# Kernel optimization log

Hardware: AMD Instinct MI355X
Metric: run time of the kernel (lower is better)

## Reference

```python
import jax, jax.numpy as jnp
import numpy as np

B, N_IN, D_IN = 2048, 49, 320
D = 768            # inner_dim
H = 8              # n_heads
DH = D // H        # head dim = 96
NQ = 8             # n_queries
D_OUT = 3072       # llama_hidden
EPS = 1e-5


def _ln(x, g, b):
    mu = jnp.mean(x, axis=-1, keepdims=True)
    var = jnp.mean(jnp.square(x - mu), axis=-1, keepdims=True)
    return (x - mu) * jax.lax.rsqrt(var + EPS) * g + b


def setup_inputs() -> dict:
    key = jax.random.key(0)
    ks = jax.random.split(key, 16)
    s = lambda k, shape, fan: jax.random.normal(k, shape, jnp.float32) * (1.0 / np.sqrt(fan))
    return {
        "features": jax.random.normal(ks[0], (B, N_IN, D_IN), jnp.float32),
        "input_proj_w": s(ks[1], (D, D_IN), D_IN),
        "input_proj_b": jnp.zeros((D,), jnp.float32),
        "queries": jax.random.normal(ks[2], (NQ, D), jnp.float32) * 0.02,
        "ln_q_g": jnp.ones((D,), jnp.float32), "ln_q_b": jnp.zeros((D,), jnp.float32),
        "ln_kv_g": jnp.ones((D,), jnp.float32), "ln_kv_b": jnp.zeros((D,), jnp.float32),
        "in_proj_w": s(ks[3], (3 * D, D), D),
        "in_proj_b": jnp.zeros((3 * D,), jnp.float32),
        "out_proj_w": s(ks[4], (D, D), D),
        "out_proj_b": jnp.zeros((D,), jnp.float32),
        "ln_ff_g": jnp.ones((D,), jnp.float32), "ln_ff_b": jnp.zeros((D,), jnp.float32),
        "ffn_w1": s(ks[5], (D, D), D), "ffn_b1": jnp.zeros((D,), jnp.float32),
        "ffn_w2": s(ks[6], (D, D), D), "ffn_b2": jnp.zeros((D,), jnp.float32),
        "output_proj_w": s(ks[7], (D_OUT, D), D),
        "output_proj_b": jnp.zeros((D_OUT,), jnp.float32),
        "final_g": jnp.ones((D_OUT,), jnp.float32), "final_b": jnp.zeros((D_OUT,), jnp.float32),
    }


def reference(features, input_proj_w, input_proj_b, queries,
              ln_q_g, ln_q_b, ln_kv_g, ln_kv_b,
              in_proj_w, in_proj_b, out_proj_w, out_proj_b,
              ln_ff_g, ln_ff_b, ffn_w1, ffn_b1, ffn_w2, ffn_b2,
              output_proj_w, output_proj_b, final_g, final_b):
    b = features.shape[0]
    # kv projection: (B, N_in, D)
    kv = jnp.einsum('bnd,ed->bne', features, input_proj_w) + input_proj_b
    q = jnp.broadcast_to(queries[None], (b, NQ, D))

    # --- single layer (n_layers=1) ---
    q_norm = _ln(q, ln_q_g, ln_q_b)
    kv_norm = _ln(kv, ln_kv_g, ln_kv_b)

    wq, wk, wv = in_proj_w[:D], in_proj_w[D:2 * D], in_proj_w[2 * D:]
    bq, bk, bv = in_proj_b[:D], in_proj_b[D:2 * D], in_proj_b[2 * D:]
    qp = (jnp.einsum('bqd,ed->bqe', q_norm, wq) + bq).reshape(b, NQ, H, DH)
    kp = (jnp.einsum('bnd,ed->bne', kv_norm, wk) + bk).reshape(b, N_IN, H, DH)
    vp = (jnp.einsum('bnd,ed->bne', kv_norm, wv) + bv).reshape(b, N_IN, H, DH)

    scores = jnp.einsum('bqhd,bnhd->bhqn', qp, kp) / np.sqrt(DH).astype(np.float32)
    attn = jax.nn.softmax(scores, axis=-1)
    ctx = jnp.einsum('bhqn,bnhd->bqhd', attn, vp).reshape(b, NQ, D)
    attn_out = jnp.einsum('bqd,ed->bqe', ctx, out_proj_w) + out_proj_b

    q = q + attn_out
    h = _ln(q, ln_ff_g, ln_ff_b)
    h = jnp.einsum('bqd,ed->bqe', h, ffn_w1) + ffn_b1
    h = jax.nn.gelu(h, approximate=False)
    h = jnp.einsum('bqd,ed->bqe', h, ffn_w2) + ffn_b2
    q = q + h

    out = jnp.einsum('bqd,ed->bqe', q, output_proj_w) + output_proj_b
    return _ln(out, final_g, final_b)
```

## Files before the change

kernel.cpp:

```cpp
#include <hip/hip_runtime.h>
#include <math.h>

typedef __attribute__((ext_vector_type(8))) short short8;
typedef __attribute__((ext_vector_type(8))) unsigned short ushort8;
typedef __attribute__((ext_vector_type(4))) float f32x4;

__device__ __forceinline__ float b2f(unsigned short h) {
    union { unsigned int u; float f; } c; c.u = ((unsigned int)h) << 16; return c.f;
}
__device__ __forceinline__ unsigned short f2b(float x) {
    union { float f; unsigned int u; } c; c.f = x;
    unsigned int r = c.u + 0x7fffu + ((c.u >> 16) & 1u);
    return (unsigned short)(r >> 16);
}

__global__ __launch_bounds__(256) void cast_all(
    const float* __restrict__ f,    unsigned short* __restrict__ fb,
    const float* __restrict__ winw, unsigned short* __restrict__ winb,
    const float* __restrict__ wv,   unsigned short* __restrict__ wvb,
    const float* __restrict__ wo,   unsigned short* __restrict__ wob,
    const float* __restrict__ w1,   unsigned short* __restrict__ w1b,
    const float* __restrict__ w2,   unsigned short* __restrict__ w2b,
    const float* __restrict__ wop,  unsigned short* __restrict__ wopb) {
    int blk = blockIdx.x;
    const float* src; unsigned short* dst; int i;
    if (blk < 31360)      { src = f;    dst = fb;   i = blk * 256 + threadIdx.x; }
    else if (blk < 31600) { src = winw; dst = winb; i = (blk - 31360) * 256 + threadIdx.x; }
    else if (blk < 32176) { src = wv;   dst = wvb;  i = (blk - 31600) * 256 + threadIdx.x; }
    else if (blk < 32752) { src = wo;   dst = wob;  i = (blk - 32176) * 256 + threadIdx.x; }
    else if (blk < 33328) { src = w1;   dst = w1b;  i = (blk - 32752) * 256 + threadIdx.x; }
    else if (blk < 33904) { src = w2;   dst = w2b;  i = (blk - 33328) * 256 + threadIdx.x; }
    else                  { src = wop;  dst = wopb; i = (blk - 33904) * 256 + threadIdx.x; }
    float4 fv = ((const float4*)src)[i];
    ushort4 o; o.x = f2b(fv.x); o.y = f2b(fv.y); o.z = f2b(fv.z); o.w = f2b(fv.w);
    ((ushort4*)dst)[i] = o;
}

template <int DD, bool INB, bool OUTB>
__global__ __launch_bounds__(256) void ln_rows(const void* __restrict__ in_, void* __restrict__ out_,
                                               const float* __restrict__ g, const float* __restrict__ bb,
                                               int nrows) {
    const int wv = threadIdx.x >> 6, l = threadIdx.x & 63;
    const int row = blockIdx.x * 4 + wv;
    if (row >= nrows) return;
    constexpr int NC = DD / 256;
    float v[DD / 64];
    if constexpr (INB) {
        const ushort4* in = (const ushort4*)((const unsigned short*)in_ + (size_t)row * DD);
#pragma unroll
        for (int c = 0; c < NC; ++c) {
            ushort4 u = in[l + 64 * c];
            v[4*c] = b2f(u.x); v[4*c+1] = b2f(u.y); v[4*c+2] = b2f(u.z); v[4*c+3] = b2f(u.w);
        }
    } else {
        const float4* in = (const float4*)((const float*)in_ + (size_t)row * DD);
#pragma unroll
        for (int c = 0; c < NC; ++c) {
            float4 u = in[l + 64 * c];
            v[4*c] = u.x; v[4*c+1] = u.y; v[4*c+2] = u.z; v[4*c+3] = u.w;
        }
    }
    float s = 0.f, s2 = 0.f;
#pragma unroll
    for (int i = 0; i < DD / 64; ++i) { s += v[i]; s2 += v[i] * v[i]; }
#pragma unroll
    for (int o = 32; o > 0; o >>= 1) { s += __shfl_xor(s, o, 64); s2 += __shfl_xor(s2, o, 64); }
    const float mu = s * (1.0f / DD);
    const float var = s2 * (1.0f / DD) - mu * mu;
    const float rs = rsqrtf(var + 1e-5f);
    if constexpr (OUTB) {
        ushort4* out = (ushort4*)((unsigned short*)out_ + (size_t)row * DD);
#pragma unroll
        for (int c = 0; c < NC; ++c) {
            int e = (l + 64 * c) * 4;
            ushort4 o4;
            o4.x = f2b((v[4*c]   - mu) * rs * g[e]   + bb[e]);
            o4.y = f2b((v[4*c+1] - mu) * rs * g[e+1] + bb[e+1]);
            o4.z = f2b((v[4*c+2] - mu) * rs * g[e+2] + bb[e+2]);
            o4.w = f2b((v[4*c+3] - mu) * rs * g[e+3] + bb[e+3]);
            out[l + 64 * c] = o4;
        }
    } else {
        float4* out = (float4*)((float*)out_ + (size_t)row * DD);
#pragma unroll
        for (int c = 0; c < NC; ++c) {
            int e = (l + 64 * c) * 4;
            float4 o4;
            o4.x = (v[4*c]   - mu) * rs * g[e]   + bb[e];
            o4.y = (v[4*c+1] - mu) * rs * g[e+1] + bb[e+1];
            o4.z = (v[4*c+2] - mu) * rs * g[e+2] + bb[e+2];
            o4.w = (v[4*c+3] - mu) * rs * g[e+3] + bb[e+3];
            out[l + 64 * c] = o4;
        }
    }
}

__global__ __launch_bounds__(256) void ln_stats(const unsigned short* __restrict__ kv,
                                                float2* __restrict__ stats, int nrows) {
    const int wv = threadIdx.x >> 6, l = threadIdx.x & 63;
    const int row = blockIdx.x * 4 + wv;
    if (row >= nrows) return;
    const ushort4* in = (const ushort4*)(kv + (size_t)row * 768);
    float s = 0.f, s2 = 0.f;
#pragma unroll
    for (int c = 0; c < 3; ++c) {
        ushort4 u = in[l + 64 * c];
        float a = b2f(u.x), b = b2f(u.y), cc = b2f(u.z), d = b2f(u.w);
        s += a + b + cc + d;
        s2 += a * a + b * b + cc * cc + d * d;
    }
#pragma unroll
    for (int o = 32; o > 0; o >>= 1) { s += __shfl_xor(s, o, 64); s2 += __shfl_xor(s2, o, 64); }
    const float mu = s * (1.0f / 768.0f);
    const float var = s2 * (1.0f / 768.0f) - mu * mu;
    const float rs = rsqrtf(var + 1e-5f);
    if (l == 0) stats[row] = make_float2(rs, rs * mu);
}

__global__ __launch_bounds__(256) void qp_kernel(const float* __restrict__ qn, const float* __restrict__ wq,
                                                 const float* __restrict__ bq, float* __restrict__ qp) {
    int q = blockIdx.x / 3;
    int col = (blockIdx.x % 3) * 256 + threadIdx.x;
    const float4* a = (const float4*)(qn + q * 768);
    const float4* wr = (const float4*)(wq + (size_t)col * 768);
    float s = 0.f;
#pragma unroll 8
    for (int k = 0; k < 192; ++k) {
        float4 xx = a[k], yy = wr[k];
        s += xx.x * yy.x + xx.y * yy.y + xx.z * yy.z + xx.w * yy.w;
    }
    qp[q * 768 + col] = s + bq[col];
}

__global__ __launch_bounds__(256) void qk_build(const float* __restrict__ qp, const float* __restrict__ wk,
                                                const float* __restrict__ g,
                                                unsigned short* __restrict__ qkg, float* __restrict__ tout) {
    __shared__ float red[4];
    const int hq = blockIdx.x, h = hq >> 3, q = hq & 7;
    const int tid = threadIdx.x;
    const float* qv = qp + q * 768 + h * 96;
    float tsum = 0.f;
#pragma unroll
    for (int c = 0; c < 3; ++c) {
        int e = tid + 256 * c;
        float s = 0.f;
        for (int d = 0; d < 96; ++d) s += qv[d] * wk[(size_t)(h * 96 + d) * 768 + e];
        unsigned short bv = f2b(s * 0.10206207262f * g[e]);
        qkg[hq * 768 + e] = bv;
        tsum += b2f(bv);
    }
#pragma unroll
    for (int o = 32; o > 0; o >>= 1) tsum += __shfl_xor(tsum, o, 64);
    if ((tid & 63) == 0) red[tid >> 6] = tsum;
    __syncthreads();
    if (tid == 0) tout[hq] = red[0] + red[1] + red[2] + red[3];
}

__device__ __forceinline__ void gll16(const void* g, void* l) {
    __builtin_amdgcn_global_load_lds((const __attribute__((address_space(1))) unsigned int*)g,
                                     (__attribute__((address_space(3))) unsigned int*)l, 16, 0, 0);
}

template <int ROWS>
__device__ __forceinline__ void stage_rows(const unsigned short* gbase, int ldg,
                                           unsigned short* lds, int tid) {
    int wuni = tid & ~63;
#pragma unroll
    for (int it = 0; it < ROWS / 32; ++it) {
        int s = it * 256 + tid;
        int r = s >> 3, c = s & 7;
        int cc = c ^ (r & 7);
        gll16(gbase + (size_t)r * ldg + cc * 8, lds + (size_t)(it * 256 + wuni) * 8);
    }
}

template <int EPI>
__global__ __launch_bounds__(256) void gemm_bf16(
    const unsigned short* __restrict__ A, const unsigned short* __restrict__ W,
    const float* __restrict__ bias, void* __restrict__ out,
    const float* __restrict__ aux, int K, int N) {
    __shared__ __align__(16) unsigned short lA[128 * 64];
    __shared__ __align__(16) unsigned short lB[128 * 64];
    const int tid = threadIdx.x;
    const int l = tid & 63, w = tid >> 6;
    int gx = gridDim.x;
    int lid = blockIdx.y * gx + blockIdx.x;
    int nwg = gx * gridDim.y;
    int idx = (nwg & 7) ? lid : ((lid & 7) * (nwg >> 3) + (lid >> 3));
    const int bm0 = (idx / gx) * 128, bn0 = (idx % gx) * 128;
    const int wm = (w >> 1) * 64, wn = (w & 1) * 64;
    const int l15 = l & 15, lk = l >> 4;
    f32x4 acc[4][4] = {};
    const int nk = K >> 6;
    const unsigned short* Abase = A + (size_t)bm0 * K;
    const unsigned short* Wbase = W + (size_t)bn0 * K;
    for (int kt = 0; kt < nk; ++kt) {
        stage_rows<128>(Abase + kt * 64, K, lA, tid);
        stage_rows<128>(Wbase + kt * 64, K, lB, tid);
        __syncthreads();
        short8 af[4], bf[4];
#pragma unroll
        for (int kk = 0; kk < 2; ++kk) {
#pragma unroll
            for (int mf = 0; mf < 4; ++mf) {
                int r = wm + mf * 16 + l15;
                int c = (kk * 4 + lk) ^ (r & 7);
                af[mf] = *(const short8*)(lA + r * 64 + c * 8);
            }
#pragma unroll
            for (int nf = 0; nf < 4; ++nf) {
                int r = wn + nf * 16 + l15;
                int c = (kk * 4 + lk) ^ (r & 7);
                bf[nf] = *(const short8*)(lB + r * 64 + c * 8);
            }
#pragma unroll
            for (int mf = 0; mf < 4; ++mf)
#pragma unroll
                for (int nf = 0; nf < 4; ++nf)
                    acc[mf][nf] = __builtin_amdgcn_mfma_f32_16x16x32_bf16(af[mf], bf[nf], acc[mf][nf], 0, 0, 0);
        }
        __syncthreads();
    }
    const int row0 = bm0 + wm + (lk << 2);
    const int col0 = bn0 + wn + l15;
#pragma unroll
    for (int nf = 0; nf < 4; ++nf) {
        int col = col0 + nf * 16;
        float bv = bias[col];
#pragma unroll
        for (int mf = 0; mf < 4; ++mf) {
#pragma unroll
            for (int r = 0; r < 4; ++r) {
                int row = row0 + mf * 16 + r;
                float v = acc[mf][nf][r] + bv;
                size_t idx2 = (size_t)row * N + col;
                if constexpr (EPI == 0) {
                    ((unsigned short*)out)[idx2] = f2b(v);
                } else if constexpr (EPI == 1) {
                    v += aux[(row & 7) * N + col];
                    ((float*)out)[idx2] = v;
                } else if constexpr (EPI == 2) {
                    v = 0.5f * v * (1.0f + erff(v * 0.70710678118f));
                    ((unsigned short*)out)[idx2] = f2b(v);
                } else if constexpr (EPI == 3) {
                    v += aux[idx2];
                    ((unsigned short*)out)[idx2] = f2b(v);
                } else {
                    ((float*)out)[idx2] = v;
                }
            }
        }
    }
}

__global__ __launch_bounds__(256) void gemm_scores(const unsigned short* __restrict__ A,
                                                   const unsigned short* __restrict__ Qk,
                                                   const float2* __restrict__ stats,
                                                   const float* __restrict__ tcol,
                                                   float* __restrict__ S) {
    __shared__ __align__(16) unsigned short lA[128 * 64];
    __shared__ __align__(16) unsigned short lB[64 * 64];
    const int tid = threadIdx.x;
    const int l = tid & 63, w = tid >> 6;
    int lid = blockIdx.x;
    int idx = (lid & 7) * (gridDim.x >> 3) + (lid >> 3);
    const int bm0 = idx * 128;
    const int wm = (w >> 1) * 64, wn = (w & 1) * 32;
    const int l15 = l & 15, lk = l >> 4;
    f32x4 acc[4][2] = {};
    const unsigned short* Abase = A + (size_t)bm0 * 768;
    for (int kt = 0; kt < 12; ++kt) {
        stage_rows<128>(Abase + kt * 64, 768, lA, tid);
        stage_rows<64>(Qk + kt * 64, 768, lB, tid);
        __syncthreads();
        short8 af[4], bf[2];
#pragma unroll
        for (int kk = 0; kk < 2; ++kk) {
#pragma unroll
            for (int mf = 0; mf < 4; ++mf) {
                int r = wm + mf * 16 + l15;
                int c = (kk * 4 + lk) ^ (r & 7);
                af[mf] = *(const short8*)(lA + r * 64 + c * 8);
            }
#pragma unroll
            for (int nf = 0; nf < 2; ++nf) {
                int r = wn + nf * 16 + l15;
                int c = (kk * 4 + lk) ^ (r & 7);
                bf[nf] = *(const short8*)(lB + r * 64 + c * 8);
            }
#pragma unroll
            for (int mf = 0; mf < 4; ++mf)
#pragma unroll
                for (int nf = 0; nf < 2; ++nf)
                    acc[mf][nf] = __builtin_amdgcn_mfma_f32_16x16x32_bf16(af[mf], bf[nf], acc[mf][nf], 0, 0, 0);
        }
        __syncthreads();
    }
    const int row0 = bm0 + wm + (lk << 2);
    const int col0 = wn + l15;
    const float tv0 = tcol[col0], tv1 = tcol[col0 + 16];
#pragma unroll
    for (int mf = 0; mf < 4; ++mf)
#pragma unroll
        for (int r = 0; r < 4; ++r) {
            int row = row0 + mf * 16 + r;
            float2 st = stats[row];
            S[(size_t)row * 64 + col0]      = st.x * acc[mf][0][r] - st.y * tv0;
            S[(size_t)row * 64 + col0 + 16] = st.x * acc[mf][1][r] - st.y * tv1;
        }
}

__global__ __launch_bounds__(256) void attn_mix(const unsigned short* __restrict__ kvr,
                                                const float* __restrict__ S,
                                                const float2* __restrict__ stats,
                                                const float* __restrict__ lg,
                                                const float* __restrict__ lb,
                                                unsigned short* __restrict__ cmix) {
    __shared__ __align__(16) unsigned short at[64 * 64];
    __shared__ __align__(16) unsigned short kvT[128 * 64];
    __shared__ float dl[64];
    float* Sl = (float*)kvT;
    const int b = blockIdx.x;
    const int t = threadIdx.x, l = t & 63, w = t >> 6;
    const int l15 = l & 15, lk = l >> 4;

    for (int i = t; i < 3136; i += 256) Sl[i] = S[(size_t)b * 3136 + i];

    const unsigned short* src = kvr + ((size_t)b * 49 + (l < 49 ? l : 0)) * 768;
    ushort8 z8 = {0, 0, 0, 0, 0, 0, 0, 0};
    ushort8 va0 = z8, va1 = z8, va2 = z8, va3 = z8;
    if (l < 49) {
        va0 = *(const ushort8*)(src + w * 8);
        va1 = *(const ushort8*)(src + w * 8 + 32);
        va2 = *(const ushort8*)(src + w * 8 + 64);
        va3 = *(const ushort8*)(src + w * 8 + 96);
    }
    __syncthreads();

    float mx = -1e30f;
    for (int n = 0; n < 49; ++n) mx = fmaxf(mx, Sl[n * 64 + l]);
    float sum = 0.f, dun = 0.f;
    for (int n = 0; n < 49; ++n) {
        float e = __expf(Sl[n * 64 + l] - mx);
        sum += e;
        dun += e * stats[(size_t)b * 49 + n].y;
    }
    float inv = 1.0f / sum;
#pragma unroll
    for (int cd = 0; cd < 2; ++cd) {
        int c = w * 2 + cd;
        int cc = c ^ (l & 7);
#pragma unroll
        for (int j = 0; j < 8; ++j) {
            int n = c * 8 + j;
            float av = 0.f;
            if (n < 49) av = __expf(Sl[n * 64 + l] - mx) * inv * stats[(size_t)b * 49 + n].x;
            at[l * 64 + cc * 8 + j] = f2b(av);
        }
    }
    if (w == 0) dl[l] = dun * inv;
    __syncthreads();

    float dls[4];
#pragma unroll
    for (int nf = 0; nf < 4; ++nf) dls[nf] = dl[nf * 16 + l15];

#pragma unroll 1
    for (int ph = 0; ph < 6; ++ph) {
#pragma unroll
        for (int i = 0; i < 4; ++i) {
            ushort8 v = (i == 0) ? va0 : (i == 1) ? va1 : (i == 2) ? va2 : va3;
            int e0 = w * 8 + i * 32;
#pragma unroll
            for (int j = 0; j < 8; ++j) {
                int e = e0 + j;
                kvT[e * 64 + (((l >> 3) ^ (e & 7)) << 3) + (l & 7)] = v[j];
            }
        }
        ushort8 nb0 = z8, nb1 = z8, nb2 = z8, nb3 = z8;
        if (ph < 5 && l < 49) {
            const unsigned short* s2 = src + (ph + 1) * 128 + w * 8;
            nb0 = *(const ushort8*)(s2);
            nb1 = *(const ushort8*)(s2 + 32);
            nb2 = *(const ushort8*)(s2 + 64);
            nb3 = *(const ushort8*)(s2 + 96);
        }
        __syncthreads();
        f32x4 acc[2][4] = {};
#pragma unroll
        for (int ks = 0; ks < 2; ++ks) {
            short8 af[2], bf[4];
#pragma unroll
            for (int mf = 0; mf < 2; ++mf) {
                int r = w * 32 + mf * 16 + l15;
                af[mf] = *(const short8*)(kvT + r * 64 + (((ks * 4 + lk) ^ (r & 7)) << 3));
            }
#pragma unroll
            for (int nf = 0; nf < 4; ++nf) {
                int r = nf * 16 + l15;
                bf[nf] = *(const short8*)(at + r * 64 + (((ks * 4 + lk) ^ (r & 7)) << 3));
            }
#pragma unroll
            for (int mf = 0; mf < 2; ++mf)
#pragma unroll
                for (int nf = 0; nf < 4; ++nf)
                    acc[mf][nf] = __builtin_amdgcn_mfma_f32_16x16x32_bf16(af[mf], bf[nf], acc[mf][nf], 0, 0, 0);
        }
#pragma unroll
        for (int mf = 0; mf < 2; ++mf) {
            int e0 = ph * 128 + w * 32 + mf * 16 + lk * 4;
            float4 g4 = *(const float4*)(lg + e0);
            float4 b4 = *(const float4*)(lb + e0);
#pragma unroll
            for (int nf = 0; nf < 4; ++nf) {
                int hq = nf * 16 + l15;
                float dv = dls[nf];
                ushort4 o;
                o.x = f2b(g4.x * (acc[mf][nf][0] - dv) + b4.x);
                o.y = f2b(g4.y * (acc[mf][nf][1] - dv) + b4.y);
                o.z = f2b(g4.z * (acc[mf][nf][2] - dv) + b4.z);
                o.w = f2b(g4.w * (acc[mf][nf][3] - dv) + b4.w);
                *(ushort4*)(cmix + ((size_t)(hq >> 3) * 16384 + b * 8 + (hq & 7)) * 768 + e0) = o;
            }
        }
        va0 = nb0; va1 = nb1; va2 = nb2; va3 = nb3;
        __syncthreads();
    }
}

__global__ __launch_bounds__(256) void gemm_ctx(const unsigned short* __restrict__ cmix,
                                                const unsigned short* __restrict__ wvb,
                                                const float* __restrict__ bv,
                                                unsigned short* __restrict__ ctx) {
    __shared__ __align__(16) unsigned short lA[128 * 64];
    __shared__ __align__(16) unsigned short lB[128 * 64];
    const int tid = threadIdx.x;
    const int l = tid & 63, w = tid >> 6;
    const int h = blockIdx.z;
    int yy = blockIdx.y;
    int idx = (yy & 7) * 16 + (yy >> 3);
    const int bm0 = idx * 128;
    const int wm = (w >> 1) * 64, wn = (w & 1) * 64;
    const int l15 = l & 15, lk = l >> 4;
    f32x4 acc[4][4] = {};
    const unsigned short* Abase = cmix + (size_t)h * 16384 * 768 + (size_t)bm0 * 768;
    const unsigned short* Wbase = wvb + (size_t)h * 96 * 768;
    for (int kt = 0; kt < 12; ++kt) {
        stage_rows<128>(Abase + kt * 64, 768, lA, tid);
        stage_rows<128>(Wbase + kt * 64, 768, lB, tid);
        __syncthreads();
        short8 af[4], bf[4];
#pragma unroll
        for (int kk = 0; kk < 2; ++kk) {
#pragma unroll
            for (int mf = 0; mf < 4; ++mf) {
                int r = wm + mf * 16 + l15;
                int c = (kk * 4 + lk) ^ (r & 7);
                af[mf] = *(const short8*)(lA + r * 64 + c * 8);
            }
#pragma unroll
            for (int nf = 0; nf < 4; ++nf) {
                int r = wn + nf * 16 + l15;
                int c = (kk * 4 + lk) ^ (r & 7);
                bf[nf] = *(const short8*)(lB + r * 64 + c * 8);
            }
#pragma unroll
            for (int mf = 0; mf < 4; ++mf)
#pragma unroll
                for (int nf = 0; nf < 4; ++nf)
                    acc[mf][nf] = __builtin_amdgcn_mfma_f32_16x16x32_bf16(af[mf], bf[nf], acc[mf][nf], 0, 0, 0);
        }
        __syncthreads();
    }
    const int row0 = bm0 + wm + (lk << 2);
    const int col0 = wn + l15;
#pragma unroll
    for (int nf = 0; nf < 4; ++nf) {
        int col = col0 + nf * 16;
        if (col >= 96) continue;
        float bvv = bv[h * 96 + col];
#pragma unroll
        for (int mf = 0; mf < 4; ++mf)
#pragma unroll
            for (int r = 0; r < 4; ++r) {
                int row = row0 + mf * 16 + r;
                ctx[(size_t)row * 768 + h * 96 + col] = f2b(acc[mf][nf][r] + bvv);
            }
    }
}

extern "C" void kernel_launch(void* const* d_in, const int* in_sizes, int n_in,
                              void* d_out, int out_size, void* d_ws, size_t ws_size,
                              hipStream_t stream) {
    (void)in_sizes; (void)n_in; (void)out_size;
    const float* features      = (const float*)d_in[0];
    const float* input_proj_w  = (const float*)d_in[1];
    const float* input_proj_b  = (const float*)d_in[2];
    const float* queries       = (const float*)d_in[3];
    const float* ln_q_g        = (const float*)d_in[4];
    const float* ln_q_b        = (const float*)d_in[5];
    const float* ln_kv_g       = (const float*)d_in[6];
    const float* ln_kv_b       = (const float*)d_in[7];
    const float* in_proj_w     = (const float*)d_in[8];
    const float* in_proj_b     = (const float*)d_in[9];
    const float* out_proj_w    = (const float*)d_in[10];
    const float* out_proj_b    = (const float*)d_in[11];
    const float* ln_ff_g       = (const float*)d_in[12];
    const float* ln_ff_b       = (const float*)d_in[13];
    const float* ffn_w1        = (const float*)d_in[14];
    const float* ffn_b1        = (const float*)d_in[15];
    const float* ffn_w2        = (const float*)d_in[16];
    const float* ffn_b2        = (const float*)d_in[17];
    const float* output_proj_w = (const float*)d_in[18];
    const float* output_proj_b = (const float*)d_in[19];
    const float* final_g       = (const float*)d_in[20];
    const float* final_b       = (const float*)d_in[21];

    char* ws = (char*)d_ws;
    size_t off = 0;
    auto alloc = [&](size_t bytes) -> char* {
        char* r = ws + off; off += (bytes + 255) & ~(size_t)255; return r;
    };
    unsigned short* featb = (unsigned short*)alloc(100352ull * 320 * 2);
    unsigned short* kvbuf = (unsigned short*)alloc(100352ull * 768 * 2);
    unsigned short* cmix  = (unsigned short*)alloc(8ull * 16384 * 768 * 2);
    float*          S     = (float*)alloc(100352ull * 64 * 4);
    float2*         stats = (float2*)alloc(100352ull * 8);
    unsigned short* winb  = (unsigned short*)alloc(768ull * 320 * 2);
    unsigned short* wvb   = (unsigned short*)alloc(768ull * 768 * 2);
    unsigned short* woutb = (unsigned short*)alloc(768ull * 768 * 2);
    unsigned short* w1b   = (unsigned short*)alloc(768ull * 768 * 2);
    unsigned short* w2b   = (unsigned short*)alloc(768ull * 768 * 2);
    unsigned short* wopb  = (unsigned short*)alloc(3072ull * 768 * 2);
    float* qnorm          = (float*)alloc(8 * 768 * 4);
    float* qpb            = (float*)alloc(8 * 768 * 4);
    unsigned short* qkb   = (unsigned short*)alloc(64ull * 768 * 2);
    float* tbuf           = (float*)alloc(64 * 4);
    if (off > ws_size) return;

    unsigned short* ctx  = featb;
    unsigned short* outb = kvbuf;
    float* x             = (float*)cmix;
    unsigned short* hn   = (unsigned short*)((char*)cmix + 50331648);
    unsigned short* f1   = (unsigned short*)((char*)cmix + 75497472);
    unsigned short* x2   = (unsigned short*)((char*)cmix + 100663296);

    cast_all<<<36208, 256, 0, stream>>>(features, featb, input_proj_w, winb,
                                        in_proj_w + 2 * 768 * 768, wvb, out_proj_w, woutb,
                                        ffn_w1, w1b, ffn_w2, w2b, output_proj_w, wopb);

    ln_rows<768, false, false><<<2, 256, 0, stream>>>(queries, qnorm, ln_q_g, ln_q_b, 8);
    qp_kernel<<<24, 256, 0, stream>>>(qnorm, in_proj_w, in_proj_b, qpb);
    qk_build<<<64, 256, 0, stream>>>(qpb, in_proj_w + 768 * 768, ln_kv_g, qkb, tbuf);

    gemm_bf16<0><<<dim3(6, 784), 256, 0, stream>>>(featb, winb, input_proj_b, kvbuf, nullptr, 320, 768);
    ln_stats<<<25088, 256, 0, stream>>>(kvbuf, stats, 100352);
    gemm_scores<<<784, 256, 0, stream>>>(kvbuf, qkb, stats, tbuf, S);
    attn_mix<<<2048, 256, 0, stream>>>(kvbuf, S, stats, ln_kv_g, ln_kv_b, cmix);
    gemm_ctx<<<dim3(1, 128, 8), 256, 0, stream>>>(cmix, wvb, in_proj_b + 1536, ctx);
    gemm_bf16<1><<<dim3(6, 128), 256, 0, stream>>>(ctx, woutb, out_proj_b, x, queries, 768, 768);
    ln_rows<768, false, true><<<4096, 256, 0, stream>>>(x, hn, ln_ff_g, ln_ff_b, 16384);
    gemm_bf16<2><<<dim3(6, 128), 256, 0, stream>>>(hn, w1b, ffn_b1, f1, nullptr, 768, 768);
    gemm_bf16<3><<<dim3(6, 128), 256, 0, stream>>>(f1, w2b, ffn_b2, x2, x, 768, 768);
    gemm_bf16<0><<<dim3(24, 128), 256, 0, stream>>>(x2, wopb, output_proj_b, outb, nullptr, 768, 3072);
    ln_rows<3072, true, false><<<4096, 256, 0, stream>>>(outb, (float*)d_out, final_g, final_b, 16384);
}
```

Baseline: 734.9 us.

## Fuse LayerNorm statistics into GEMM epilogues and fold FFN LN into W1

```diff
diff --git a/kernel.cpp b/kernel.cpp
--- a/kernel.cpp
+++ b/kernel.cpp
@@ -21,7 +21,8 @@
     const float* __restrict__ wo,   unsigned short* __restrict__ wob,
     const float* __restrict__ w1,   unsigned short* __restrict__ w1b,
     const float* __restrict__ w2,   unsigned short* __restrict__ w2b,
-    const float* __restrict__ wop,  unsigned short* __restrict__ wopb) {
+    const float* __restrict__ wop,  unsigned short* __restrict__ wopb,
+    const float* __restrict__ gff) {
     int blk = blockIdx.x;
     const float* src; unsigned short* dst; int i;
     if (blk < 31360)      { src = f;    dst = fb;   i = blk * 256 + threadIdx.x; }
@@ -32,6 +33,10 @@
     else if (blk < 33904) { src = w2;   dst = w2b;  i = (blk - 33328) * 256 + threadIdx.x; }
     else                  { src = wop;  dst = wopb; i = (blk - 33904) * 256 + threadIdx.x; }
     float4 fv = ((const float4*)src)[i];
+    if (blk >= 32752 && blk < 33328) {
+        float4 g4 = ((const float4*)gff)[i % 192];
+        fv.x *= g4.x; fv.y *= g4.y; fv.z *= g4.z; fv.w *= g4.w;
+    }
     ushort4 o; o.x = f2b(fv.x); o.y = f2b(fv.y); o.z = f2b(fv.z); o.w = f2b(fv.w);
     ((ushort4*)dst)[i] = o;
 }
@@ -95,28 +100,6 @@
     }
 }
 
-__global__ __launch_bounds__(256) void ln_stats(const unsigned short* __restrict__ kv,
-                                                float2* __restrict__ stats, int nrows) {
-    const int wv = threadIdx.x >> 6, l = threadIdx.x & 63;
-    const int row = blockIdx.x * 4 + wv;
-    if (row >= nrows) return;
-    const ushort4* in = (const ushort4*)(kv + (size_t)row * 768);
-    float s = 0.f, s2 = 0.f;
-#pragma unroll
-    for (int c = 0; c < 3; ++c) {
-        ushort4 u = in[l + 64 * c];
-        float a = b2f(u.x), b = b2f(u.y), cc = b2f(u.z), d = b2f(u.w);
-        s += a + b + cc + d;
-        s2 += a * a + b * b + cc * cc + d * d;
-    }
-#pragma unroll
-    for (int o = 32; o > 0; o >>= 1) { s += __shfl_xor(s, o, 64); s2 += __shfl_xor(s2, o, 64); }
-    const float mu = s * (1.0f / 768.0f);
-    const float var = s2 * (1.0f / 768.0f) - mu * mu;
-    const float rs = rsqrtf(var + 1e-5f);
-    if (l == 0) stats[row] = make_float2(rs, rs * mu);
-}
-
 __global__ __launch_bounds__(256) void qp_kernel(const float* __restrict__ qn, const float* __restrict__ wq,
                                                  const float* __restrict__ bq, float* __restrict__ qp) {
     int q = blockIdx.x / 3;
@@ -156,6 +139,24 @@
     if (tid == 0) tout[hq] = red[0] + red[1] + red[2] + red[3];
 }
 
+__global__ __launch_bounds__(256) void t1c1_build(const float* __restrict__ w1, const float* __restrict__ g,
+                                                  const float* __restrict__ beta, const float* __restrict__ b1,
+                                                  float* __restrict__ tvec, float* __restrict__ fb1) {
+    int col = blockIdx.x * 256 + threadIdx.x;
+    const float4* wr = (const float4*)(w1 + (size_t)col * 768);
+    const float4* g4 = (const float4*)g;
+    const float4* be = (const float4*)beta;
+    float st = 0.f, sc = 0.f;
+#pragma unroll 8
+    for (int k = 0; k < 192; ++k) {
+        float4 w = wr[k], gg = g4[k], bb = be[k];
+        st += w.x * gg.x + w.y * gg.y + w.z * gg.z + w.w * gg.w;
+        sc += w.x * bb.x + w.y * bb.y + w.z * bb.z + w.w * bb.w;
+    }
+    tvec[col] = st;
+    fb1[col] = sc + b1[col];
+}
+
 __device__ __forceinline__ void gll16(const void* g, void* l) {
     __builtin_amdgcn_global_load_lds((const __attribute__((address_space(1))) unsigned int*)g,
                                      (__attribute__((address_space(3))) unsigned int*)l, 16, 0, 0);
@@ -174,20 +175,31 @@
     }
 }
 
-template <int EPI>
+template <int EPI, bool STATS>
 __global__ __launch_bounds__(256) void gemm_bf16(
     const unsigned short* __restrict__ A, const unsigned short* __restrict__ W,
     const float* __restrict__ bias, void* __restrict__ out,
-    const float* __restrict__ aux, int K, int N) {
+    const void* __restrict__ aux, const float2* __restrict__ rstats,
+    float2* __restrict__ statsout, const float* __restrict__ tvec,
+    int K, int N, int CG) {
     __shared__ __align__(16) unsigned short lA[128 * 64];
     __shared__ __align__(16) unsigned short lB[128 * 64];
     const int tid = threadIdx.x;
     const int l = tid & 63, w = tid >> 6;
-    int gx = gridDim.x;
+    int gx = gridDim.x, gy = gridDim.y;
     int lid = blockIdx.y * gx + blockIdx.x;
-    int nwg = gx * gridDim.y;
-    int idx = (nwg & 7) ? lid : ((lid & 7) * (nwg >> 3) + (lid >> 3));
-    const int bm0 = (idx / gx) * 128, bn0 = (idx % gx) * 128;
+    int nwg = gx * gy;
+    int bm0, bn0;
+    if ((nwg & 7) || (gy & 7)) {
+        bm0 = (lid / gx) * 128; bn0 = (lid % gx) * 128;
+    } else {
+        int xcd = lid & 7, loc = lid >> 3;
+        int rpx = gy >> 3;
+        int perg = rpx * CG;
+        int cg = loc / perg, rem = loc % perg;
+        bm0 = (xcd * rpx + rem / CG) * 128;
+        bn0 = (cg * CG + rem % CG) * 128;
+    }
     const int wm = (w >> 1) * 64, wn = (w & 1) * 64;
     const int l15 = l & 15, lk = l >> 4;
     f32x4 acc[4][4] = {};
@@ -223,30 +235,53 @@
     }
     const int row0 = bm0 + wm + (lk << 2);
     const int col0 = bn0 + wn + l15;
+    float bv[4], tv[4];
 #pragma unroll
     for (int nf = 0; nf < 4; ++nf) {
-        int col = col0 + nf * 16;
-        float bv = bias[col];
-#pragma unroll
-        for (int mf = 0; mf < 4; ++mf) {
-#pragma unroll
-            for (int r = 0; r < 4; ++r) {
-                int row = row0 + mf * 16 + r;
-                float v = acc[mf][nf][r] + bv;
+        bv[nf] = bias[col0 + nf * 16];
+        if constexpr (EPI == 2) tv[nf] = tvec[col0 + nf * 16];
+    }
+#pragma unroll
+    for (int mf = 0; mf < 4; ++mf) {
+#pragma unroll
+        for (int r = 0; r < 4; ++r) {
+            int row = row0 + mf * 16 + r;
+            float rs = 0.f, u = 0.f;
+            if constexpr (EPI == 2) {
+                float2 sm = rstats[row];
+                float mu = sm.x * (1.0f / 768.0f);
+                float var = sm.y * (1.0f / 768.0f) - mu * mu;
+                rs = rsqrtf(var + 1e-5f);
+                u = rs * mu;
+            }
+            float smv = 0.f, smv2 = 0.f;
+#pragma unroll
+            for (int nf = 0; nf < 4; ++nf) {
+                int col = col0 + nf * 16;
                 size_t idx2 = (size_t)row * N + col;
+                float v = acc[mf][nf][r];
                 if constexpr (EPI == 0) {
-                    ((unsigned short*)out)[idx2] = f2b(v);
+                    v += bv[nf];
                 } else if constexpr (EPI == 1) {
-                    v += aux[(row & 7) * N + col];
-                    ((float*)out)[idx2] = v;
+                    v += bv[nf] + ((const float*)aux)[(row & 7) * N + col];
                 } else if constexpr (EPI == 2) {
+                    v = rs * v - u * tv[nf] + bv[nf];
                     v = 0.5f * v * (1.0f + erff(v * 0.70710678118f));
-                    ((unsigned short*)out)[idx2] = f2b(v);
-                } else if constexpr (EPI == 3) {
-                    v += aux[idx2];
-                    ((unsigned short*)out)[idx2] = f2b(v);
                 } else {
-                    ((float*)out)[idx2] = v;
+                    v += bv[nf] + b2f(((const unsigned short*)aux)[idx2]);
+                }
+                if constexpr (STATS) { smv += v; smv2 += v * v; }
+                ((unsigned short*)out)[idx2] = f2b(v);
+            }
+            if constexpr (STATS) {
+#pragma unroll
+                for (int o = 8; o > 0; o >>= 1) {
+                    smv += __shfl_xor(smv, o, 64);
+                    smv2 += __shfl_xor(smv2, o, 64);
+                }
+                if (l15 == 0) {
+                    atomicAdd(&((float*)statsout)[row * 2], smv);
+                    atomicAdd(&((float*)statsout)[row * 2 + 1], smv2);
                 }
             }
         }
@@ -304,9 +339,13 @@
 #pragma unroll
         for (int r = 0; r < 4; ++r) {
             int row = row0 + mf * 16 + r;
-            float2 st = stats[row];
-            S[(size_t)row * 64 + col0]      = st.x * acc[mf][0][r] - st.y * tv0;
-            S[(size_t)row * 64 + col0 + 16] = st.x * acc[mf][1][r] - st.y * tv1;
+            float2 sm = stats[row];
+            float mu = sm.x * (1.0f / 768.0f);
+            float var = sm.y * (1.0f / 768.0f) - mu * mu;
+            float rs = rsqrtf(var + 1e-5f);
+            float u = rs * mu;
+            S[(size_t)row * 64 + col0]      = rs * acc[mf][0][r] - u * tv0;
+            S[(size_t)row * 64 + col0 + 16] = rs * acc[mf][1][r] - u * tv1;
         }
 }
 
@@ -319,12 +358,20 @@
     __shared__ __align__(16) unsigned short at[64 * 64];
     __shared__ __align__(16) unsigned short kvT[128 * 64];
     __shared__ float dl[64];
+    __shared__ float2 sst[49];
     float* Sl = (float*)kvT;
     const int b = blockIdx.x;
     const int t = threadIdx.x, l = t & 63, w = t >> 6;
     const int l15 = l & 15, lk = l >> 4;
 
     for (int i = t; i < 3136; i += 256) Sl[i] = S[(size_t)b * 3136 + i];
+    if (t < 49) {
+        float2 sm = stats[(size_t)b * 49 + t];
+        float mu = sm.x * (1.0f / 768.0f);
+        float var = sm.y * (1.0f / 768.0f) - mu * mu;
+        float rs = rsqrtf(var + 1e-5f);
+        sst[t] = make_float2(rs, rs * mu);
+    }
 
     const unsigned short* src = kvr + ((size_t)b * 49 + (l < 49 ? l : 0)) * 768;
     ushort8 z8 = {0, 0, 0, 0, 0, 0, 0, 0};
@@ -343,7 +390,7 @@
     for (int n = 0; n < 49; ++n) {
         float e = __expf(Sl[n * 64 + l] - mx);
         sum += e;
-        dun += e * stats[(size_t)b * 49 + n].y;
+        dun += e * sst[n].y;
     }
     float inv = 1.0f / sum;
 #pragma unroll
@@ -354,7 +401,7 @@
         for (int j = 0; j < 8; ++j) {
             int n = c * 8 + j;
             float av = 0.f;
-            if (n < 49) av = __expf(Sl[n * 64 + l] - mx) * inv * stats[(size_t)b * 49 + n].x;
+            if (n < 49) av = __expf(Sl[n * 64 + l] - mx) * inv * sst[n].x;
             at[l * 64 + cc * 8 + j] = f2b(av);
         }
     }
@@ -525,43 +572,52 @@
     unsigned short* kvbuf = (unsigned short*)alloc(100352ull * 768 * 2);
     unsigned short* cmix  = (unsigned short*)alloc(8ull * 16384 * 768 * 2);
     float*          S     = (float*)alloc(100352ull * 64 * 4);
-    float2*         stats = (float2*)alloc(100352ull * 8);
+    float2*         kvst  = (float2*)alloc(100352ull * 8);
+    float2*         xst   = (float2*)alloc(16384ull * 8);
     unsigned short* winb  = (unsigned short*)alloc(768ull * 320 * 2);
     unsigned short* wvb   = (unsigned short*)alloc(768ull * 768 * 2);
     unsigned short* woutb = (unsigned short*)alloc(768ull * 768 * 2);
-    unsigned short* w1b   = (unsigned short*)alloc(768ull * 768 * 2);
+    unsigned short* w1gb  = (unsigned short*)alloc(768ull * 768 * 2);
     unsigned short* w2b   = (unsigned short*)alloc(768ull * 768 * 2);
     unsigned short* wopb  = (unsigned short*)alloc(3072ull * 768 * 2);
     float* qnorm          = (float*)alloc(8 * 768 * 4);
     float* qpb            = (float*)alloc(8 * 768 * 4);
     unsigned short* qkb   = (unsigned short*)alloc(64ull * 768 * 2);
     float* tbuf           = (float*)alloc(64 * 4);
+    float* t1vec          = (float*)alloc(768 * 4);
+    float* fb1            = (float*)alloc(768 * 4);
     if (off > ws_size) return;
 
     unsigned short* ctx  = featb;
     unsigned short* outb = kvbuf;
-    float* x             = (float*)cmix;
-    unsigned short* hn   = (unsigned short*)((char*)cmix + 50331648);
-    unsigned short* f1   = (unsigned short*)((char*)cmix + 75497472);
-    unsigned short* x2   = (unsigned short*)((char*)cmix + 100663296);
+    unsigned short* xb   = (unsigned short*)cmix;
+    unsigned short* f1   = (unsigned short*)((char*)cmix + 25165824);
+    unsigned short* x2   = (unsigned short*)((char*)cmix + 50331648);
+
+    hipMemsetAsync(kvst, 0, 100352ull * 8, stream);
+    hipMemsetAsync(xst, 0, 16384ull * 8, stream);
 
     cast_all<<<36208, 256, 0, stream>>>(features, featb, input_proj_w, winb,
                                         in_proj_w + 2 * 768 * 768, wvb, out_proj_w, woutb,
-                                        ffn_w1, w1b, ffn_w2, w2b, output_proj_w, wopb);
+                                        ffn_w1, w1gb, ffn_w2, w2b, output_proj_w, wopb, ln_ff_g);
 
     ln_rows<768, false, false><<<2, 256, 0, stream>>>(queries, qnorm, ln_q_g, ln_q_b, 8);
     qp_kernel<<<24, 256, 0, stream>>>(qnorm, in_proj_w, in_proj_b, qpb);
     qk_build<<<64, 256, 0, stream>>>(qpb, in_proj_w + 768 * 768, ln_kv_g, qkb, tbuf);
-
-    gemm_bf16<0><<<dim3(6, 784), 256, 0, stream>>>(featb, winb, input_proj_b, kvbuf, nullptr, 320, 768);
-    ln_stats<<<25088, 256, 0, stream>>>(kvbuf, stats, 100352);
-    gemm_scores<<<784, 256, 0, stream>>>(kvbuf, qkb, stats, tbuf, S);
-    attn_mix<<<2048, 256, 0, stream>>>(kvbuf, S, stats, ln_kv_g, ln_kv_b, cmix);
+    t1c1_build<<<3, 256, 0, stream>>>(ffn_w1, ln_ff_g, ln_ff_b, ffn_b1, t1vec, fb1);
+
+    gemm_bf16<0, true><<<dim3(6, 784), 256, 0, stream>>>(featb, winb, input_proj_b, kvbuf,
+                                                         nullptr, nullptr, kvst, nullptr, 320, 768, 6);
+    gemm_scores<<<784, 256, 0, stream>>>(kvbuf, qkb, kvst, tbuf, S);
+    attn_mix<<<2048, 256, 0, stream>>>(kvbuf, S, kvst, ln_kv_g, ln_kv_b, cmix);
     gemm_ctx<<<dim3(1, 128, 8), 256, 0, stream>>>(cmix, wvb, in_proj_b + 1536, ctx);
-    gemm_bf16<1><<<dim3(6, 128), 256, 0, stream>>>(ctx, woutb, out_proj_b, x, queries, 768, 768);
-    ln_rows<768, false, true><<<4096, 256, 0, stream>>>(x, hn, ln_ff_g, ln_ff_b, 16384);
-    gemm_bf16<2><<<dim3(6, 128), 256, 0, stream>>>(hn, w1b, ffn_b1, f1, nullptr, 768, 768);
-    gemm_bf16<3><<<dim3(6, 128), 256, 0, stream>>>(f1, w2b, ffn_b2, x2, x, 768, 768);
-    gemm_bf16<0><<<dim3(24, 128), 256, 0, stream>>>(x2, wopb, output_proj_b, outb, nullptr, 768, 3072);
+    gemm_bf16<1, true><<<dim3(6, 128), 256, 0, stream>>>(ctx, woutb, out_proj_b, xb,
+                                                         queries, nullptr, xst, nullptr, 768, 768, 6);
+    gemm_bf16<2, false><<<dim3(6, 128), 256, 0, stream>>>(xb, w1gb, fb1, f1,
+                                                          nullptr, xst, nullptr, t1vec, 768, 768, 6);
+    gemm_bf16<3, false><<<dim3(6, 128), 256, 0, stream>>>(f1, w2b, ffn_b2, x2,
+                                                          xb, nullptr, nullptr, nullptr, 768, 768, 6);
+    gemm_bf16<0, false><<<dim3(24, 128), 256, 0, stream>>>(x2, wopb, output_proj_b, outb,
+                                                           nullptr, nullptr, nullptr, nullptr, 768, 3072, 12);
     ln_rows<3072, true, false><<<4096, 256, 0, stream>>>(outb, (float*)d_out, final_g, final_b, 16384);
 }
```

After: 803.2 us. +9.3%, slower.
